# Performance work log

Measured on AMD Instinct MI355X. Metric: run time of the kernel, lower is better.

Reference implementation:

```python
import jax, jax.numpy as jnp
import numpy as np

N = 100000
E = 800000
HID = 512
HEADS = 8
F = HID // HEADS  # 64


def setup_inputs() -> dict:
    key = jax.random.key(0)
    k = jax.random.split(key, 8)
    in_nodes_features = jax.random.normal(k[0], (N, HID), dtype=jnp.float32)
    edge_index = jax.random.randint(k[1], (2, E), 0, N, dtype=jnp.int64)
    # xavier_normal gain=1.414 for W: std = gain * sqrt(2/(fan_in+fan_out))
    std_w = 1.414 * np.sqrt(2.0 / (HID + HID))
    W = jax.random.normal(k[2], (HID, HID), dtype=jnp.float32) * std_w
    b_lin = jnp.zeros((HID,), dtype=jnp.float32)
    std_s = 1.414 * np.sqrt(2.0 / (HEADS + F))  # xavier on (1,H,F) treats fan dims loosely; use per-slice
    a_src = jax.random.normal(k[3], (1, HEADS, F), dtype=jnp.float32) * std_s
    a_tgt = jax.random.normal(k[4], (1, HEADS, F), dtype=jnp.float32) * std_s
    bias = jnp.zeros((HID,), dtype=jnp.float32)
    prelu_a = jnp.asarray(0.25, dtype=jnp.float32)  # PReLU default init
    return {
        "in_nodes_features": in_nodes_features,
        "edge_index": edge_index,
        "W": W,
        "b_lin": b_lin,
        "a_src": a_src,
        "a_tgt": a_tgt,
        "bias": bias,
        "prelu_a": prelu_a,
    }


def reference(in_nodes_features, edge_index, W, b_lin, a_src, a_tgt, bias, prelu_a):
    num_nodes = in_nodes_features.shape[0]
    src, trg = edge_index[0], edge_index[1]

    # projection: [N, HID] -> [N, HEADS, F]
    proj = (in_nodes_features @ W.T + b_lin).reshape(num_nodes, HEADS, F)

    # per-node attention scores [N, HEADS]
    scores_source = jnp.sum(proj * a_src, axis=-1)
    scores_target = jnp.sum(proj * a_tgt, axis=-1)

    # lift to edges and score: [E, HEADS]
    scores_per_edge = jax.nn.leaky_relu(
        scores_source[src] + scores_target[trg], negative_slope=0.01
    )

    # neighborhood-aware softmax (global max subtraction as in original)
    exp_scores = jnp.exp(scores_per_edge - jnp.max(scores_per_edge))
    denom = jax.ops.segment_sum(exp_scores, trg, num_segments=num_nodes)  # [N, HEADS]
    attn = exp_scores / (denom[trg] + 1e-16)  # [E, HEADS]

    # weighted aggregation: [E, HEADS, F] scatter-add -> [N, HEADS, F]
    weighted = proj[src] * attn[:, :, None]
    out = jax.ops.segment_sum(weighted, trg, num_segments=num_nodes)
    out = out.reshape(num_nodes, HID) + bias

    # PReLU with single shared parameter
    return jnp.where(out >= 0, out, prelu_a * out)
```

## Files before the change

### kernel.cpp

```cpp
#include <hip/hip_runtime.h>
#include <stdint.h>

#define N_NODES 100000
#define N_EDGES 800000
#define HIDDIM 512
#define HEADS 8
#define FDIM 64

typedef __attribute__((ext_vector_type(4))) float f32x4;
typedef __attribute__((ext_vector_type(8))) short short8;
typedef __attribute__((ext_vector_type(8))) unsigned short ushort8;

static constexpr size_t OFF_PROJ   = 0;
static constexpr size_t OFF_SSRC   = 102400000;
static constexpr size_t OFF_STGT   = 105600000;
static constexpr size_t OFF_COUNTS = 108800000;
static constexpr size_t OFF_CURSOR = 109200000;
static constexpr size_t OFF_KEYS   = 109600000;
static constexpr size_t OFF_ROWOFF = 109600016;
static constexpr size_t OFF_BSUM   = 110000016;
static constexpr size_t OFF_SSORT  = 110004112;
static constexpr size_t OFF_WB     = 113204112;

__device__ __forceinline__ unsigned short f2bf(float f) {
  unsigned int u = __builtin_bit_cast(unsigned int, f);
  u += 0x7FFFu + ((u >> 16) & 1u);
  return (unsigned short)(u >> 16);
}
__device__ __forceinline__ float bf2f(unsigned short s) {
  unsigned int u = ((unsigned int)s) << 16;
  return __builtin_bit_cast(float, u);
}
__device__ __forceinline__ unsigned int fkey(float x) {
  unsigned int b = __builtin_bit_cast(unsigned int, x);
  return (b & 0x80000000u) ? ~b : (b | 0x80000000u);
}
__device__ __forceinline__ float fdec(unsigned int k) {
  unsigned int b = (k & 0x80000000u) ? (k & 0x7FFFFFFFu) : ~k;
  return __builtin_bit_cast(float, b);
}
__device__ __forceinline__ void gload_lds16(const void* g, void* l) {
  __builtin_amdgcn_global_load_lds((const __attribute__((address_space(1))) unsigned int*)g,
                                   (__attribute__((address_space(3))) unsigned int*)l, 16, 0, 0);
}

__global__ __launch_bounds__(256) void prep(const float* __restrict__ W,
                                            unsigned short* __restrict__ Wb,
                                            unsigned int* __restrict__ zbase) {
  int i = blockIdx.x * 256 + threadIdx.x;
  if (i < 32768) {
    const float4 v0 = *(const float4*)&W[(size_t)i * 8];
    const float4 v1 = *(const float4*)&W[(size_t)i * 8 + 4];
    ushort8 u;
    u[0] = f2bf(v0.x); u[1] = f2bf(v0.y); u[2] = f2bf(v0.z); u[3] = f2bf(v0.w);
    u[4] = f2bf(v1.x); u[5] = f2bf(v1.y); u[6] = f2bf(v1.z); u[7] = f2bf(v1.w);
    *(ushort8*)&Wb[(size_t)i * 8] = u;
  }
  if (i < 200004) zbase[i] = 0;
}

__global__ __launch_bounds__(512) void gemm_proj(
    const float* __restrict__ X, const unsigned short* __restrict__ Wb,
    const float* __restrict__ b_lin, const float* __restrict__ a_src,
    const float* __restrict__ a_tgt, const int* __restrict__ ei,
    int* __restrict__ counts,
    unsigned short* __restrict__ proj, float* __restrict__ s_src,
    float* __restrict__ s_tgt, unsigned int* __restrict__ keys) {
  __shared__ __align__(16) unsigned short Al[128 * 64];
  __shared__ __align__(16) unsigned short Bl[256 * 64];
  __shared__ float red[16];
  const int t = threadIdx.x;
  const int id = blockIdx.x;
  const int q = id >> 4, bn = (id >> 3) & 1, r = id & 7;
  const int bm = q * 8 + r;
  const int lane = t & 63, wid = t >> 6;
  const int wr = wid >> 2, wc = wid & 3;

  {
    int e = id * 512 + t;
    if (e < N_EDGES) atomicAdd(&counts[ei[N_EDGES + e]], 1);
  }
  if (bm >= 782) return;

  f32x4 acc[4][4] = {};

  const int brow0 = bn * 256 + wid * 32 + (lane >> 3);
  const int bsrc_c = ((lane & 7) ^ (lane >> 3)) * 8;

  for (int kt = 0; kt < 8; ++kt) {
#pragma unroll
    for (int i = 0; i < 4; ++i)
      gload_lds16(&Wb[(size_t)(brow0 + i * 8) * 512 + kt * 64 + bsrc_c],
                  &Bl[(wid * 4 + i) * 512]);
#pragma unroll
    for (int i = 0; i < 2; ++i) {
      int idx8 = i * 512 + t;
      int row = idx8 >> 3, ck = idx8 & 7;
      int grow = bm * 128 + row;
      if (grow >= N_NODES) grow = N_NODES - 1;
      const float4 v0 = *(const float4*)&X[(size_t)grow * 512 + kt * 64 + ck * 8];
      const float4 v1 = *(const float4*)&X[(size_t)grow * 512 + kt * 64 + ck * 8 + 4];
      ushort8 u;
      u[0] = f2bf(v0.x); u[1] = f2bf(v0.y); u[2] = f2bf(v0.z); u[3] = f2bf(v0.w);
      u[4] = f2bf(v1.x); u[5] = f2bf(v1.y); u[6] = f2bf(v1.z); u[7] = f2bf(v1.w);
      *(ushort8*)&Al[row * 64 + ((ck ^ (row & 7)) * 8)] = u;
    }
    __syncthreads();
#pragma unroll
    for (int kk = 0; kk < 2; ++kk) {
      short8 af[4], bfr[4];
#pragma unroll
      for (int i = 0; i < 4; ++i) {
        int row = wr * 64 + i * 16 + (lane & 15);
        int ck = (kk * 4 + (lane >> 4)) ^ (row & 7);
        af[i] = *(const short8*)&Al[row * 64 + ck * 8];
      }
#pragma unroll
      for (int j = 0; j < 4; ++j) {
        int row = wc * 64 + j * 16 + (lane & 15);
        int ck = (kk * 4 + (lane >> 4)) ^ (row & 7);
        bfr[j] = *(const short8*)&Bl[row * 64 + ck * 8];
      }
#pragma unroll
      for (int i = 0; i < 4; ++i)
#pragma unroll
        for (int j = 0; j < 4; ++j)
          acc[i][j] = __builtin_amdgcn_mfma_f32_16x16x32_bf16(af[i], bfr[j], acc[i][j], 0, 0, 0);
    }
    __syncthreads();
  }

  const int col_head_base = bn * 256 + wc * 64;
  const int h = col_head_base >> 6;
  float asr[4], atg[4], bl[4];
#pragma unroll
  for (int j = 0; j < 4; ++j) {
    int f = j * 16 + (lane & 15);
    asr[j] = a_src[h * FDIM + f];
    atg[j] = a_tgt[h * FDIM + f];
    bl[j] = b_lin[col_head_base + f];
  }
  float wms = -1e30f, wmt = -1e30f;
#pragma unroll
  for (int i = 0; i < 4; ++i) {
#pragma unroll
    for (int rr = 0; rr < 4; ++rr) {
      int grow = bm * 128 + wr * 64 + i * 16 + (lane >> 4) * 4 + rr;
      float v[4];
      float ps = 0.f, pt = 0.f;
#pragma unroll
      for (int j = 0; j < 4; ++j) {
        v[j] = acc[i][j][rr] + bl[j];
        ps += v[j] * asr[j];
        pt += v[j] * atg[j];
      }
#pragma unroll
      for (int m = 1; m < 16; m <<= 1) {
        ps += __shfl_xor(ps, m);
        pt += __shfl_xor(pt, m);
      }
      wms = fmaxf(wms, ps);
      wmt = fmaxf(wmt, pt);
      if (grow < N_NODES) {
#pragma unroll
        for (int j = 0; j < 4; ++j)
          proj[(size_t)grow * 512 + col_head_base + j * 16 + (lane & 15)] = f2bf(v[j]);
        if ((lane & 15) == 0) {
          s_src[grow * HEADS + h] = ps;
          s_tgt[grow * HEADS + h] = pt;
        }
      }
    }
  }
#pragma unroll
  for (int m = 16; m < 64; m <<= 1) {
    wms = fmaxf(wms, __shfl_xor(wms, m));
    wmt = fmaxf(wmt, __shfl_xor(wmt, m));
  }
  if (lane == 0) { red[wid] = wms; red[8 + wid] = wmt; }
  __syncthreads();
  if (t == 0) {
    float ms = red[0], mt = red[8];
#pragma unroll
    for (int i = 1; i < 8; ++i) { ms = fmaxf(ms, red[i]); mt = fmaxf(mt, red[8 + i]); }
    atomicMax(&keys[0], fkey(ms));
    atomicMax(&keys[1], fkey(mt));
  }
}

__global__ void scan1(const int* __restrict__ counts, int* __restrict__ row_off,
                      int* __restrict__ bsum) {
  __shared__ int sh[256];
  int t = threadIdx.x, i = blockIdx.x * 256 + t;
  int v = (i < N_NODES) ? counts[i] : 0;
  sh[t] = v;
  __syncthreads();
  for (int off = 1; off < 256; off <<= 1) {
    int x = (t >= off) ? sh[t - off] : 0;
    __syncthreads();
    sh[t] += x;
    __syncthreads();
  }
  if (i < N_NODES) row_off[i] = sh[t] - v;
  if (t == 255) bsum[blockIdx.x] = sh[255];
}
__global__ void scan2(int* __restrict__ bsum, int nb) {
  __shared__ int sh[512];
  int t = threadIdx.x;
  int v = (t < nb) ? bsum[t] : 0;
  sh[t] = v;
  __syncthreads();
  for (int off = 1; off < 512; off <<= 1) {
    int x = (t >= off) ? sh[t - off] : 0;
    __syncthreads();
    sh[t] += x;
    __syncthreads();
  }
  if (t < nb) bsum[t] = sh[t] - v;
}

__global__ void edge_pass2(const int* __restrict__ ei, const int* __restrict__ row_off,
                           const int* __restrict__ bsum, int* __restrict__ cursor,
                           int* __restrict__ sorted_src) {
  int e = blockIdx.x * 256 + threadIdx.x;
  if (e >= N_EDGES) return;
  int src = ei[e], trg = ei[N_EDGES + e];
  int pos = row_off[trg] + bsum[trg >> 8] + atomicAdd(&cursor[trg], 1);
  sorted_src[pos] = src;
}

__global__ __launch_bounds__(256) void aggregate(
    const int* __restrict__ row_off, const int* __restrict__ bsum,
    const int* __restrict__ counts, const int* __restrict__ sorted_src,
    const float* __restrict__ s_src, const float* __restrict__ s_tgt,
    const unsigned int* __restrict__ keys, const unsigned short* __restrict__ proj,
    const float* __restrict__ bias, const float* __restrict__ prelu_a,
    float* __restrict__ out) {
  const int node = blockIdx.x * 4 + (threadIdx.x >> 6);
  if (node >= N_NODES) return;
  const int lane = threadIdx.x & 63;
  const int h = lane >> 3;
  const int f8 = (lane & 7) * 8;
  const int start = row_off[node] + bsum[node >> 8];
  const int deg = counts[node];
  const float st = s_tgt[node * HEADS + h];
  const float M = fmaxf(0.0f, fdec(keys[0]) + fdec(keys[1]));

  float acc[8] = {};
  float dsum = 0.f;
  for (int jb = 0; jb < deg; jb += 8) {
    const int nb = deg - jb;
    int s[8];
#pragma unroll
    for (int i = 0; i < 8; ++i) s[i] = sorted_src[start + jb + (i < nb ? i : 0)];
    float x[8];
#pragma unroll
    for (int i = 0; i < 8; ++i) x[i] = s_src[s[i] * HEADS + h];
    ushort8 p[8];
#pragma unroll
    for (int i = 0; i < 8; ++i)
      p[i] = *(const ushort8*)&proj[(size_t)s[i] * 512 + h * 64 + f8];
#pragma unroll
    for (int i = 0; i < 8; ++i) {
      if (i < nb) {
        float xx = x[i] + st;
        float l = xx > 0.f ? xx : 0.01f * xx;
        float e = __expf(l - M);
        dsum += e;
#pragma unroll
        for (int k = 0; k < 8; ++k) acc[k] += e * bf2f(p[i][k]);
      }
    }
  }
  const float inv = 1.0f / (dsum + 1e-16f);
  const float pa = prelu_a[0];
  const int c = h * 64 + f8;
  float o[8];
#pragma unroll
  for (int k = 0; k < 8; ++k) {
    float v = acc[k] * inv + bias[c + k];
    o[k] = v >= 0.f ? v : pa * v;
  }
  float4* op = (float4*)&out[(size_t)node * 512 + c];
  op[0] = make_float4(o[0], o[1], o[2], o[3]);
  op[1] = make_float4(o[4], o[5], o[6], o[7]);
}

extern "C" void kernel_launch(void* const* d_in, const int* in_sizes, int n_in,
                              void* d_out, int out_size, void* d_ws, size_t ws_size,
                              hipStream_t stream) {
  const float* X = (const float*)d_in[0];
  const int* ei = (const int*)d_in[1];
  const float* W = (const float*)d_in[2];
  const float* b_lin = (const float*)d_in[3];
  const float* a_src = (const float*)d_in[4];
  const float* a_tgt = (const float*)d_in[5];
  const float* bias = (const float*)d_in[6];
  const float* prelu_a = (const float*)d_in[7];

  char* ws = (char*)d_ws;
  unsigned short* proj = (unsigned short*)(ws + OFF_PROJ);
  float* s_src = (float*)(ws + OFF_SSRC);
  float* s_tgt = (float*)(ws + OFF_STGT);
  int* counts = (int*)(ws + OFF_COUNTS);
  int* cursor = (int*)(ws + OFF_CURSOR);
  unsigned int* keys = (unsigned int*)(ws + OFF_KEYS);
  int* row_off = (int*)(ws + OFF_ROWOFF);
  int* bsum = (int*)(ws + OFF_BSUM);
  int* sorted_src = (int*)(ws + OFF_SSORT);
  unsigned short* Wb = (unsigned short*)(ws + OFF_WB);

  prep<<<3125, 256, 0, stream>>>(W, Wb, (unsigned int*)(ws + OFF_COUNTS));
  gemm_proj<<<1568, 512, 0, stream>>>(X, Wb, b_lin, a_src, a_tgt, ei, counts,
                                      proj, s_src, s_tgt, keys);
  scan1<<<391, 256, 0, stream>>>(counts, row_off, bsum);
  scan2<<<1, 512, 0, stream>>>(bsum, 391);
  edge_pass2<<<3125, 256, 0, stream>>>(ei, row_off, bsum, cursor, sorted_src);
  aggregate<<<25000, 256, 0, stream>>>(row_off, bsum, counts, sorted_src, s_src, s_tgt, keys,
                                       proj, bias, prelu_a, (float*)d_out);
}
```

Measured before the change: 352.3 us.

## Load GEMM B tiles directly to registers with double buffering; drop cursor array

The GEMM stops staging the bf16 weight tile through LDS with global_load_lds and instead has each wave load its B fragments straight into registers, double-buffered so the next k-tile's loads overlap the current MFMA work. The edge bucketing reuses row_off itself as the atomic cursor instead of a separate cursor array, and aggregate recovers the start offset by subtracting the degree. Together these cut LDS traffic, drop one zeroing pass, and shrink the prep grid. The cost is higher register pressure from two 8-entry short8 buffers and redundant global or L2 reads of W across the waves that share columns.

Result: slower. 433.3 us (+23.0%).

```diff
diff --git a/kernel.cpp b/kernel.cpp
--- a/kernel.cpp
+++ b/kernel.cpp
@@ -15,7 +15,6 @@
 static constexpr size_t OFF_SSRC   = 102400000;
 static constexpr size_t OFF_STGT   = 105600000;
 static constexpr size_t OFF_COUNTS = 108800000;
-static constexpr size_t OFF_CURSOR = 109200000;
 static constexpr size_t OFF_KEYS   = 109600000;
 static constexpr size_t OFF_ROWOFF = 109600016;
 static constexpr size_t OFF_BSUM   = 110000016;
@@ -39,14 +38,11 @@
   unsigned int b = (k & 0x80000000u) ? (k & 0x7FFFFFFFu) : ~k;
   return __builtin_bit_cast(float, b);
 }
-__device__ __forceinline__ void gload_lds16(const void* g, void* l) {
-  __builtin_amdgcn_global_load_lds((const __attribute__((address_space(1))) unsigned int*)g,
-                                   (__attribute__((address_space(3))) unsigned int*)l, 16, 0, 0);
-}
 
 __global__ __launch_bounds__(256) void prep(const float* __restrict__ W,
                                             unsigned short* __restrict__ Wb,
-                                            unsigned int* __restrict__ zbase) {
+                                            unsigned int* __restrict__ counts_z,
+                                            unsigned int* __restrict__ keys_z) {
   int i = blockIdx.x * 256 + threadIdx.x;
   if (i < 32768) {
     const float4 v0 = *(const float4*)&W[(size_t)i * 8];
@@ -56,7 +52,8 @@
     u[4] = f2bf(v1.x); u[5] = f2bf(v1.y); u[6] = f2bf(v1.z); u[7] = f2bf(v1.w);
     *(ushort8*)&Wb[(size_t)i * 8] = u;
   }
-  if (i < 200004) zbase[i] = 0;
+  if (i < N_NODES) counts_z[i] = 0;
+  if (i < 4) keys_z[i] = 0;
 }
 
 __global__ __launch_bounds__(512) void gemm_proj(
@@ -67,7 +64,6 @@
     unsigned short* __restrict__ proj, float* __restrict__ s_src,
     float* __restrict__ s_tgt, unsigned int* __restrict__ keys) {
   __shared__ __align__(16) unsigned short Al[128 * 64];
-  __shared__ __align__(16) unsigned short Bl[256 * 64];
   __shared__ float red[16];
   const int t = threadIdx.x;
   const int id = blockIdx.x;
@@ -84,51 +80,70 @@
 
   f32x4 acc[4][4] = {};
 
-  const int brow0 = bn * 256 + wid * 32 + (lane >> 3);
-  const int bsrc_c = ((lane & 7) ^ (lane >> 3)) * 8;
-
-  for (int kt = 0; kt < 8; ++kt) {
-#pragma unroll
-    for (int i = 0; i < 4; ++i)
-      gload_lds16(&Wb[(size_t)(brow0 + i * 8) * 512 + kt * 64 + bsrc_c],
-                  &Bl[(wid * 4 + i) * 512]);
-#pragma unroll
-    for (int i = 0; i < 2; ++i) {
-      int idx8 = i * 512 + t;
-      int row = idx8 >> 3, ck = idx8 & 7;
-      int grow = bm * 128 + row;
-      if (grow >= N_NODES) grow = N_NODES - 1;
-      const float4 v0 = *(const float4*)&X[(size_t)grow * 512 + kt * 64 + ck * 8];
-      const float4 v1 = *(const float4*)&X[(size_t)grow * 512 + kt * 64 + ck * 8 + 4];
-      ushort8 u;
-      u[0] = f2bf(v0.x); u[1] = f2bf(v0.y); u[2] = f2bf(v0.z); u[3] = f2bf(v0.w);
-      u[4] = f2bf(v1.x); u[5] = f2bf(v1.y); u[6] = f2bf(v1.z); u[7] = f2bf(v1.w);
-      *(ushort8*)&Al[row * 64 + ((ck ^ (row & 7)) * 8)] = u;
-    }
-    __syncthreads();
-#pragma unroll
-    for (int kk = 0; kk < 2; ++kk) {
-      short8 af[4], bfr[4];
-#pragma unroll
-      for (int i = 0; i < 4; ++i) {
-        int row = wr * 64 + i * 16 + (lane & 15);
-        int ck = (kk * 4 + (lane >> 4)) ^ (row & 7);
-        af[i] = *(const short8*)&Al[row * 64 + ck * 8];
-      }
-#pragma unroll
-      for (int j = 0; j < 4; ++j) {
-        int row = wc * 64 + j * 16 + (lane & 15);
-        int ck = (kk * 4 + (lane >> 4)) ^ (row & 7);
-        bfr[j] = *(const short8*)&Bl[row * 64 + ck * 8];
-      }
-#pragma unroll
-      for (int i = 0; i < 4; ++i)
-#pragma unroll
-        for (int j = 0; j < 4; ++j)
-          acc[i][j] = __builtin_amdgcn_mfma_f32_16x16x32_bf16(af[i], bfr[j], acc[i][j], 0, 0, 0);
-    }
-    __syncthreads();
-  }
+  const unsigned short* wbBase =
+      Wb + (size_t)(bn * 256 + wc * 64 + (lane & 15)) * 512 + (lane >> 4) * 8;
+
+  short8 bregA[8], bregB[8];
+
+#define LOADB(dst, kt)                                                          \
+  {                                                                             \
+    _Pragma("unroll") for (int j = 0; j < 4; ++j)                               \
+        _Pragma("unroll") for (int kk = 0; kk < 2; ++kk)                        \
+            dst[j * 2 + kk] =                                                   \
+                *(const short8*)(wbBase + (size_t)j * 16 * 512 + (kt) * 64 + kk * 32); \
+  }
+#define STAGE_A(kt)                                                             \
+  {                                                                             \
+    _Pragma("unroll") for (int i = 0; i < 2; ++i) {                             \
+      int idx8 = i * 512 + t;                                                   \
+      int row = idx8 >> 3, ck = idx8 & 7;                                       \
+      int grow = bm * 128 + row;                                                \
+      if (grow >= N_NODES) grow = N_NODES - 1;                                  \
+      const float4 v0 = *(const float4*)&X[(size_t)grow * 512 + (kt) * 64 + ck * 8]; \
+      const float4 v1 = *(const float4*)&X[(size_t)grow * 512 + (kt) * 64 + ck * 8 + 4]; \
+      ushort8 u;                                                                \
+      u[0] = f2bf(v0.x); u[1] = f2bf(v0.y); u[2] = f2bf(v0.z); u[3] = f2bf(v0.w); \
+      u[4] = f2bf(v1.x); u[5] = f2bf(v1.y); u[6] = f2bf(v1.z); u[7] = f2bf(v1.w); \
+      *(ushort8*)&Al[row * 64 + ((ck ^ (row & 7)) * 8)] = u;                    \
+    }                                                                           \
+  }
+#define COMPUTE(CUR)                                                            \
+  {                                                                             \
+    _Pragma("unroll") for (int kk = 0; kk < 2; ++kk) {                          \
+      short8 af[4];                                                             \
+      _Pragma("unroll") for (int i = 0; i < 4; ++i) {                           \
+        int row = wr * 64 + i * 16 + (lane & 15);                               \
+        int ck = (kk * 4 + (lane >> 4)) ^ (row & 7);                            \
+        af[i] = *(const short8*)&Al[row * 64 + ck * 8];                         \
+      }                                                                         \
+      _Pragma("unroll") for (int i = 0; i < 4; ++i)                             \
+          _Pragma("unroll") for (int j = 0; j < 4; ++j)                         \
+              acc[i][j] = __builtin_amdgcn_mfma_f32_16x16x32_bf16(              \
+                  af[i], CUR[j * 2 + kk], acc[i][j], 0, 0, 0);                  \
+    }                                                                           \
+  }
+#define STEP(kt, CUR, NXT)                                                      \
+  {                                                                             \
+    if ((kt) < 7) LOADB(NXT, (kt) + 1);   \
+    STAGE_A(kt);                                                                \
+    __syncthreads();                                                            \
+    COMPUTE(CUR);                                                               \
+    __syncthreads();                                                            \
+  }
+
+  LOADB(bregA, 0);
+  STEP(0, bregA, bregB);
+  STEP(1, bregB, bregA);
+  STEP(2, bregA, bregB);
+  STEP(3, bregB, bregA);
+  STEP(4, bregA, bregB);
+  STEP(5, bregB, bregA);
+  STEP(6, bregA, bregB);
+  STEP(7, bregB, bregA);
+#undef LOADB
+#undef STAGE_A
+#undef COMPUTE
+#undef STEP
 
   const int col_head_base = bn * 256 + wc * 64;
   const int h = col_head_base >> 6;
@@ -219,13 +234,12 @@
   if (t < nb) bsum[t] = sh[t] - v;
 }
 
-__global__ void edge_pass2(const int* __restrict__ ei, const int* __restrict__ row_off,
-                           const int* __restrict__ bsum, int* __restrict__ cursor,
-                           int* __restrict__ sorted_src) {
+__global__ void edge_pass2(const int* __restrict__ ei, int* __restrict__ row_off,
+                           const int* __restrict__ bsum, int* __restrict__ sorted_src) {
   int e = blockIdx.x * 256 + threadIdx.x;
   if (e >= N_EDGES) return;
   int src = ei[e], trg = ei[N_EDGES + e];
-  int pos = row_off[trg] + bsum[trg >> 8] + atomicAdd(&cursor[trg], 1);
+  int pos = atomicAdd(&row_off[trg], 1) + bsum[trg >> 8];
   sorted_src[pos] = src;
 }
 
@@ -241,8 +255,8 @@
   const int lane = threadIdx.x & 63;
   const int h = lane >> 3;
   const int f8 = (lane & 7) * 8;
-  const int start = row_off[node] + bsum[node >> 8];
   const int deg = counts[node];
+  const int start = row_off[node] - deg + bsum[node >> 8];
   const float st = s_tgt[node * HEADS + h];
   const float M = fmaxf(0.0f, fdec(keys[0]) + fdec(keys[1]));
 
@@ -303,19 +317,19 @@
   float* s_src = (float*)(ws + OFF_SSRC);
   float* s_tgt = (float*)(ws + OFF_STGT);
   int* counts = (int*)(ws + OFF_COUNTS);
-  int* cursor = (int*)(ws + OFF_CURSOR);
   unsigned int* keys = (unsigned int*)(ws + OFF_KEYS);
   int* row_off = (int*)(ws + OFF_ROWOFF);
   int* bsum = (int*)(ws + OFF_BSUM);
   int* sorted_src = (int*)(ws + OFF_SSORT);
   unsigned short* Wb = (unsigned short*)(ws + OFF_WB);
 
-  prep<<<3125, 256, 0, stream>>>(W, Wb, (unsigned int*)(ws + OFF_COUNTS));
+  prep<<<391, 256, 0, stream>>>(W, Wb, (unsigned int*)(ws + OFF_COUNTS),
+                                (unsigned int*)(ws + OFF_KEYS));
   gemm_proj<<<1568, 512, 0, stream>>>(X, Wb, b_lin, a_src, a_tgt, ei, counts,
                                       proj, s_src, s_tgt, keys);
   scan1<<<391, 256, 0, stream>>>(counts, row_off, bsum);
   scan2<<<1, 512, 0, stream>>>(bsum, 391);
-  edge_pass2<<<3125, 256, 0, stream>>>(ei, row_off, bsum, cursor, sorted_src);
+  edge_pass2<<<3125, 256, 0, stream>>>(ei, row_off, bsum, sorted_src);
   aggregate<<<25000, 256, 0, stream>>>(row_off, bsum, counts, sorted_src, s_src, s_tgt, keys,
                                        proj, bias, prelu_a, (float*)d_out);
 }
```
